# Kernel optimization log

Hardware: AMD Instinct MI355X
Metric: run time of the kernel (lower is better)

Reference implementation:

```python
import jax, jax.numpy as jnp
import numpy as np

N = 100000
E = 1600000
HID = 128
EPS = 1e-8


def _linear_params(key, fan_in, fan_out, bias=True, gain=1.0):
    kw, kb = jax.random.split(key)
    bound = gain / np.sqrt(fan_in)
    W = jax.random.uniform(kw, (fan_in, fan_out), jnp.float32, -bound, bound)
    if bias:
        b = jax.random.uniform(kb, (fan_out,), jnp.float32, -bound, bound)
        return W, b
    return W


def setup_inputs() -> dict:
    key = jax.random.key(0)
    ks = jax.random.split(key, 12)
    h = jax.random.normal(ks[0], (N, HID), jnp.float32)
    coord = jax.random.normal(ks[1], (N, 3), jnp.float32)
    edge_index = jax.random.randint(ks[2], (2, E), 0, N, jnp.int64)
    # edge_mlp: Linear(2*HID+1 -> HID), SiLU, Linear(HID -> HID), SiLU
    We1, be1 = _linear_params(ks[3], 2 * HID + 1, HID)
    We2, be2 = _linear_params(ks[4], HID, HID)
    # node_mlp: Linear(2*HID -> HID), SiLU, Linear(HID -> HID)
    Wn1, bn1 = _linear_params(ks[5], 2 * HID, HID)
    Wn2, bn2 = _linear_params(ks[6], HID, HID)
    # coord_mlp: Linear(HID -> HID), SiLU, Linear(HID -> 1, no bias, xavier gain=0.001)
    Wc1, bc1 = _linear_params(ks[7], HID, HID)
    Wc2 = _linear_params(ks[8], HID, 1, bias=False, gain=0.001 * np.sqrt(6.0 * HID / (HID + 1)))
    return {
        "h": h, "edge_index": edge_index, "coord": coord,
        "We1": We1, "be1": be1, "We2": We2, "be2": be2,
        "Wn1": Wn1, "bn1": bn1, "Wn2": Wn2, "bn2": bn2,
        "Wc1": Wc1, "bc1": bc1, "Wc2": Wc2,
    }


def _egcl(h, edge_index, coord, We1, be1, We2, be2, Wn1, bn1, Wn2, bn2, Wc1, bc1, Wc2):
    row, col = edge_index[0], edge_index[1]
    n = h.shape[0]
    # coord2radial (normalize=True, detach on norm)
    coord_diff = coord[row] - coord[col]                       # [E,3]
    radial = jnp.sum(coord_diff ** 2, axis=1, keepdims=True)   # [E,1]
    norm = jax.lax.stop_gradient(jnp.sqrt(radial)) + EPS
    coord_diff = coord_diff / norm
    # edge_model (no edge_attr, no attention)
    edge_in = jnp.concatenate([h[row], h[col], radial], axis=1)  # [E, 2H+1]
    m = jax.nn.silu(edge_in @ We1 + be1)
    m = jax.nn.silu(m @ We2 + be2)                               # [E,H]
    # coord_model (coords_agg='mean', tanh=False)
    phi_x = jax.nn.silu(m @ Wc1 + bc1) @ Wc2                     # [E,1]
    trans = coord_diff * phi_x                                   # [E,3]
    agg_c = jax.ops.segment_sum(trans, row, num_segments=n)
    cnt = jax.ops.segment_sum(jnp.ones((trans.shape[0],), trans.dtype), row, num_segments=n)
    agg_c = agg_c / jnp.clip(cnt, 1.0, None)[:, None]
    coord_out = coord + agg_c
    # node_model (residual=True)
    agg_h = jax.ops.segment_sum(m, row, num_segments=n)          # [N,H]
    node_in = jnp.concatenate([h, agg_h], axis=1)
    out = jax.nn.silu(node_in @ Wn1 + bn1) @ Wn2 + bn2
    h_out = h + out
    return h_out, coord_out


def reference(h, edge_index, coord, We1, be1, We2, be2, Wn1, bn1, Wn2, bn2, Wc1, bc1, Wc2):
    return _egcl(h, edge_index, coord, We1, be1, We2, be2, Wn1, bn1, Wn2, bn2, Wc1, bc1, Wc2)
```

## Files before the change

kernel.cpp:

```cpp
#include <hip/hip_runtime.h>

#define NN 100000
#define NE 1600000
#define HD 128
#define EPSV 1e-8f
#define EB 64
#define LPAD 136

typedef unsigned short ushort_t;
typedef __attribute__((ext_vector_type(8))) short bf16x8;
typedef __attribute__((ext_vector_type(4))) float f32x4;

__device__ __forceinline__ float silu_f(float x) {
    return x * __builtin_amdgcn_rcpf(1.0f + __expf(-x));
}
__device__ __forceinline__ float b2f(unsigned short u) {
    union { unsigned int i; float f; } v; v.i = ((unsigned int)u) << 16; return v.f;
}
__device__ __forceinline__ unsigned short f2b(float f) {
    union { float f; unsigned int i; } v; v.f = f;
    unsigned int r = v.i + 0x7fff + ((v.i >> 16) & 1);
    return (unsigned short)(r >> 16);
}
__device__ __forceinline__ unsigned int cvt_pk_bf16(float lo, float hi) {
    unsigned int r;
    asm("v_cvt_pk_bf16_f32 %0, %1, %2" : "=v"(r) : "v"(lo), "v"(hi));
    return r;
}
__device__ __forceinline__ bf16x8 frag_from_f32(const float* p) {
    float4 a0 = *(const float4*)p;
    float4 a1 = *(const float4*)(p + 4);
    union { bf16x8 v; uint4 u; } r;
    r.u.x = cvt_pk_bf16(a0.x, a0.y); r.u.y = cvt_pk_bf16(a0.z, a0.w);
    r.u.z = cvt_pk_bf16(a1.x, a1.y); r.u.w = cvt_pk_bf16(a1.z, a1.w);
    return r.v;
}

extern "C" __global__ __launch_bounds__(256)
void k_prep_hist(const int* __restrict__ ei, int* __restrict__ deg,
                 const float* __restrict__ We2, const float* __restrict__ Wc1,
                 const float* __restrict__ We1, const float* __restrict__ Wn1,
                 const float* __restrict__ Wn2,
                 ushort_t* __restrict__ We2T, ushort_t* __restrict__ Wc1T,
                 ushort_t* __restrict__ WabT, ushort_t* __restrict__ Wn1T,
                 ushort_t* __restrict__ Wn2T)
{
    int id = blockIdx.x * 256 + threadIdx.x;
    atomicAdd(&deg[ei[id]], 1);
    if (id < 16384) {
        int n = id >> 7, k = id & 127;
        We2T[id] = f2b(We2[k * HD + n]);
    } else if (id < 32768) {
        int r = id - 16384; int n = r >> 7, k = r & 127;
        Wc1T[r] = f2b(Wc1[k * HD + n]);
    } else if (id < 65536) {
        int r = id - 32768; int j = r >> 7, k = r & 127;
        float v = (j < 128) ? We1[k * HD + j] : We1[(size_t)(128 + k) * HD + (j - 128)];
        WabT[r] = f2b(v);
    } else if (id < 98304) {
        int r = id - 65536; int j = r >> 8, k = r & 255;
        Wn1T[r] = f2b(Wn1[(size_t)k * HD + j]);
    } else if (id < 114688) {
        int r = id - 98304; int j = r >> 7, k = r & 127;
        Wn2T[r] = f2b(Wn2[k * HD + j]);
    }
}

extern "C" __global__ __launch_bounds__(1024)
void k_scan1(const int* __restrict__ deg, int* __restrict__ bsum)
{
    __shared__ int wsum[16];
    const int tid = threadIdx.x;
    const int lane = tid & 63, w = tid >> 6;
    int i = blockIdx.x * 1024 + tid;
    int v = (i < NN) ? deg[i] : 0;
#pragma unroll
    for (int off = 32; off > 0; off >>= 1) v += __shfl_xor(v, off, 64);
    if (lane == 0) wsum[w] = v;
    __syncthreads();
    if (tid == 0) {
        int s = 0;
#pragma unroll
        for (int k = 0; k < 16; k++) s += wsum[k];
        bsum[blockIdx.x] = s;
    }
}

extern "C" __global__ __launch_bounds__(1024)
void k_scan3(const int* __restrict__ deg, const int* __restrict__ bsum,
             int* __restrict__ cursor)
{
    __shared__ int wsum[16];
    __shared__ int boff_s;
    const int tid = threadIdx.x;
    const int lane = tid & 63, w = tid >> 6;
    int i = blockIdx.x * 1024 + tid;
    int v = (i < NN) ? deg[i] : 0;
    int s = v;
#pragma unroll
    for (int off = 1; off < 64; off <<= 1) {
        int t = __shfl_up(s, off, 64);
        if (lane >= off) s += t;
    }
    if (lane == 63) wsum[w] = s;
    if (w == 0) {
        int a = 0;
        for (int k = lane; k < blockIdx.x; k += 64) a += bsum[k];
#pragma unroll
        for (int off = 32; off > 0; off >>= 1) a += __shfl_xor(a, off, 64);
        if (lane == 0) boff_s = a;
    }
    __syncthreads();
    if (w == 0) {
        int ws = (lane < 16) ? wsum[lane] : 0;
#pragma unroll
        for (int off = 1; off < 16; off <<= 1) {
            int t = __shfl_up(ws, off, 64);
            if (lane >= off) ws += t;
        }
        if (lane < 16) wsum[lane] = ws;
    }
    __syncthreads();
    int excl = boff_s + ((w > 0) ? wsum[w - 1] : 0) + s - v;
    if (i < NN) cursor[i] = excl;
}

extern "C" __global__ __launch_bounds__(256)
void k_sortids(const int* __restrict__ ei, int* __restrict__ cursor,
               int2* __restrict__ rc)
{
    int e = blockIdx.x * 256 + threadIdx.x;
    int r = ei[e], c = ei[NE + e];
    int slot = atomicAdd(&cursor[r], 1);
    rc[slot] = make_int2(r, c);
}

extern "C" __global__ __launch_bounds__(256)
void k_ab(const float* __restrict__ h, const ushort_t* __restrict__ WabT,
          const float* __restrict__ be1,
          ushort_t* __restrict__ A, ushort_t* __restrict__ B)
{
    const int tid = threadIdx.x;
    const int n0 = blockIdx.x * 64;
    const int wave = tid >> 6, lane = tid & 63;
    const int lr = lane & 15, lg = lane >> 4;
    const int node = n0 + wave * 16 + lr;
    const int nsrc = (node < NN) ? node : (NN - 1);

    f32x4 acc[16];
#pragma unroll
    for (int nt = 0; nt < 16; nt++) acc[nt] = (f32x4){0.f, 0.f, 0.f, 0.f};
#pragma unroll
    for (int ks = 0; ks < 4; ks++) {
        bf16x8 hf8 = frag_from_f32(h + (size_t)nsrc * HD + ks * 32 + lg * 8);
#pragma unroll
        for (int nt = 0; nt < 16; nt++) {
            bf16x8 wf = *(const bf16x8*)(WabT + (size_t)(nt * 16 + lr) * HD + ks * 32 + lg * 8);
            acc[nt] = __builtin_amdgcn_mfma_f32_16x16x32_bf16(wf, hf8, acc[nt], 0, 0, 0);
        }
    }
    if (node < NN) {
#pragma unroll
        for (int nt = 0; nt < 16; nt++) {
            float4 bias = (nt < 8) ? ((const float4*)be1)[nt * 4 + lg]
                                   : (float4){0.f, 0.f, 0.f, 0.f};
            uint2 pk;
            pk.x = cvt_pk_bf16(acc[nt][0] + bias.x, acc[nt][1] + bias.y);
            pk.y = cvt_pk_bf16(acc[nt][2] + bias.z, acc[nt][3] + bias.w);
            if (nt < 8)
                *(uint2*)(A + (size_t)node * HD + nt * 16 + lg * 4) = pk;
            else
                *(uint2*)(B + (size_t)node * HD + (nt - 8) * 16 + lg * 4) = pk;
        }
    }
}

extern "C" __global__ __launch_bounds__(256, 4)
void k_edge(const int2* __restrict__ rc, const float* __restrict__ coord,
            const ushort_t* __restrict__ A, const ushort_t* __restrict__ B,
            const float* __restrict__ WeL, const float* __restrict__ be2,
            const ushort_t* __restrict__ We2T,
            const ushort_t* __restrict__ Wc1T,
            const float* __restrict__ bc1, const float* __restrict__ Wc2,
            float* __restrict__ agg_h, float* __restrict__ agg_c)
{
    __shared__ ushort_t m_lds[EB][LPAD] __attribute__((aligned(16)));
    __shared__ float cd_lds[EB][3];
    __shared__ int rows_s[EB];
    __shared__ float bias_lds[384] __attribute__((aligned(16)));
    __shared__ float wel_lds[128] __attribute__((aligned(16)));

    const int tid = threadIdx.x;
    const int e  = tid >> 2;
    const int q  = tid & 3;
    const int wave = tid >> 6, lane = tid & 63;
    const int lr = lane & 15, lg = lane >> 4;

    if (tid < 128) { bias_lds[tid] = be2[tid]; bias_lds[256 + tid] = Wc2[tid]; }
    else           { bias_lds[tid] = bc1[tid - 128]; wel_lds[tid - 128] = WeL[tid - 128]; }

    int2 rce = rc[blockIdx.x * EB + e];
    const int row = rce.x, col = rce.y;

    float c0 = coord[(size_t)row * 3 + 0] - coord[(size_t)col * 3 + 0];
    float c1 = coord[(size_t)row * 3 + 1] - coord[(size_t)col * 3 + 1];
    float c2 = coord[(size_t)row * 3 + 2] - coord[(size_t)col * 3 + 2];
    float radial = c0 * c0 + c1 * c1 + c2 * c2;
    if (q == 0) {
        rows_s[e] = row;
        float inv = __builtin_amdgcn_rcpf(sqrtf(radial) + EPSV);
        cd_lds[e][0] = c0 * inv; cd_lds[e][1] = c1 * inv; cd_lds[e][2] = c2 * inv;
    }
    __syncthreads();

    {
        const bf16x8* A8 = (const bf16x8*)(A + (size_t)row * HD + q * 32);
        const bf16x8* B8 = (const bf16x8*)(B + (size_t)col * HD + q * 32);
        const float4* WL4 = (const float4*)wel_lds + q * 8;
#pragma unroll
        for (int i = 0; i < 4; i++) {
            bf16x8 av = A8[i], bv = B8[i];
            float4 w0 = WL4[2 * i], w1 = WL4[2 * i + 1];
            float v0 = silu_f(b2f((ushort_t)av[0]) + b2f((ushort_t)bv[0]) + radial * w0.x);
            float v1 = silu_f(b2f((ushort_t)av[1]) + b2f((ushort_t)bv[1]) + radial * w0.y);
            float v2 = silu_f(b2f((ushort_t)av[2]) + b2f((ushort_t)bv[2]) + radial * w0.z);
            float v3 = silu_f(b2f((ushort_t)av[3]) + b2f((ushort_t)bv[3]) + radial * w0.w);
            float v4 = silu_f(b2f((ushort_t)av[4]) + b2f((ushort_t)bv[4]) + radial * w1.x);
            float v5 = silu_f(b2f((ushort_t)av[5]) + b2f((ushort_t)bv[5]) + radial * w1.y);
            float v6 = silu_f(b2f((ushort_t)av[6]) + b2f((ushort_t)bv[6]) + radial * w1.z);
            float v7 = silu_f(b2f((ushort_t)av[7]) + b2f((ushort_t)bv[7]) + radial * w1.w);
            uint4 p;
            p.x = cvt_pk_bf16(v0, v1); p.y = cvt_pk_bf16(v2, v3);
            p.z = cvt_pk_bf16(v4, v5); p.w = cvt_pk_bf16(v6, v7);
            *(uint4*)&m_lds[e][q * 32 + i * 8] = p;
        }
    }
    __syncthreads();

    if (wave < 2) {
        f32x4 acc[2][8];
#pragma unroll
        for (int mt = 0; mt < 2; mt++)
#pragma unroll
            for (int nt = 0; nt < 8; nt++) acc[mt][nt] = (f32x4){0.f, 0.f, 0.f, 0.f};
#pragma unroll
        for (int ks = 0; ks < 4; ks++) {
            bf16x8 mf0 = *(const bf16x8*)&m_lds[wave * 32 + lr][ks * 32 + lg * 8];
            bf16x8 mf1 = *(const bf16x8*)&m_lds[wave * 32 + 16 + lr][ks * 32 + lg * 8];
#pragma unroll
            for (int nt = 0; nt < 8; nt++) {
                bf16x8 wf = *(const bf16x8*)(We2T + (size_t)(nt * 16 + lr) * HD + ks * 32 + lg * 8);
                acc[0][nt] = __builtin_amdgcn_mfma_f32_16x16x32_bf16(wf, mf0, acc[0][nt], 0, 0, 0);
                acc[1][nt] = __builtin_amdgcn_mfma_f32_16x16x32_bf16(wf, mf1, acc[1][nt], 0, 0, 0);
            }
        }
#pragma unroll
        for (int nt = 0; nt < 8; nt++) {
            float4 be2v = *(const float4*)&bias_lds[nt * 16 + lg * 4];
#pragma unroll
            for (int mt = 0; mt < 2; mt++) {
                float v0 = silu_f(acc[mt][nt][0] + be2v.x);
                float v1 = silu_f(acc[mt][nt][1] + be2v.y);
                float v2 = silu_f(acc[mt][nt][2] + be2v.z);
                float v3 = silu_f(acc[mt][nt][3] + be2v.w);
                uint2 pk; pk.x = cvt_pk_bf16(v0, v1); pk.y = cvt_pk_bf16(v2, v3);
                *(uint2*)&m_lds[wave * 32 + mt * 16 + lr][nt * 16 + lg * 4] = pk;
            }
        }

#pragma unroll
        for (int mt = 0; mt < 2; mt++)
#pragma unroll
            for (int nt = 0; nt < 8; nt++) acc[mt][nt] = (f32x4){0.f, 0.f, 0.f, 0.f};
#pragma unroll
        for (int ks = 0; ks < 4; ks++) {
            bf16x8 mf0 = *(const bf16x8*)&m_lds[wave * 32 + lr][ks * 32 + lg * 8];
            bf16x8 mf1 = *(const bf16x8*)&m_lds[wave * 32 + 16 + lr][ks * 32 + lg * 8];
#pragma unroll
            for (int nt = 0; nt < 8; nt++) {
                bf16x8 wf = *(const bf16x8*)(Wc1T + (size_t)(nt * 16 + lr) * HD + ks * 32 + lg * 8);
                acc[0][nt] = __builtin_amdgcn_mfma_f32_16x16x32_bf16(wf, mf0, acc[0][nt], 0, 0, 0);
                acc[1][nt] = __builtin_amdgcn_mfma_f32_16x16x32_bf16(wf, mf1, acc[1][nt], 0, 0, 0);
            }
        }

        float ph0 = 0.f, ph1 = 0.f;
#pragma unroll
        for (int nt = 0; nt < 8; nt++) {
            float4 bc1v = *(const float4*)&bias_lds[128 + nt * 16 + lg * 4];
            float4 wc2v = *(const float4*)&bias_lds[256 + nt * 16 + lg * 4];
            ph0 += silu_f(acc[0][nt][0] + bc1v.x) * wc2v.x
                 + silu_f(acc[0][nt][1] + bc1v.y) * wc2v.y
                 + silu_f(acc[0][nt][2] + bc1v.z) * wc2v.z
                 + silu_f(acc[0][nt][3] + bc1v.w) * wc2v.w;
            ph1 += silu_f(acc[1][nt][0] + bc1v.x) * wc2v.x
                 + silu_f(acc[1][nt][1] + bc1v.y) * wc2v.y
                 + silu_f(acc[1][nt][2] + bc1v.z) * wc2v.z
                 + silu_f(acc[1][nt][3] + bc1v.w) * wc2v.w;
        }
        ph0 += __shfl_xor(ph0, 16, 64); ph0 += __shfl_xor(ph0, 32, 64);
        ph1 += __shfl_xor(ph1, 16, 64); ph1 += __shfl_xor(ph1, 32, 64);
        if (lg == 0) {
            int e0 = wave * 32 + lr, e1 = e0 + 16;
            cd_lds[e0][0] *= ph0; cd_lds[e0][1] *= ph0; cd_lds[e0][2] *= ph0;
            cd_lds[e1][0] *= ph1; cd_lds[e1][1] *= ph1; cd_lds[e1][2] *= ph1;
        }
    }

    __syncthreads();

    {
        const int j = tid & 127, g = tid >> 7;
        const int es0 = g * 32, es1 = es0 + 32;
        float acc_r = 0.f;
        int cur = rows_s[es0];
        for (int es = es0; es < es1; es++) {
            int r = rows_s[es];
            if (r != cur) {
                atomicAdd(&agg_h[(size_t)cur * HD + j], acc_r);
                acc_r = 0.f; cur = r;
            }
            acc_r += b2f(m_lds[es][j]);
        }
        atomicAdd(&agg_h[(size_t)cur * HD + j], acc_r);
    }
    if (wave == 0) {
        int c = lane >> 4, sub = lane & 15;
        if (c < 3) {
            const int es0 = sub * 4, es1 = es0 + 4;
            float acc_r = 0.f;
            int cur = rows_s[es0];
            for (int es = es0; es < es1; es++) {
                int r = rows_s[es];
                if (r != cur) {
                    atomicAdd(&agg_c[(size_t)cur * 3 + c], acc_r);
                    acc_r = 0.f; cur = r;
                }
                acc_r += cd_lds[es][c];
            }
            atomicAdd(&agg_c[(size_t)cur * 3 + c], acc_r);
        }
    }
}

extern "C" __global__ __launch_bounds__(256)
void k_node(const float* __restrict__ h, const ushort_t* __restrict__ Wn1T,
            const float* __restrict__ bn1, const ushort_t* __restrict__ Wn2T,
            const float* __restrict__ bn2, const float* __restrict__ coord,
            const int* __restrict__ deg,
            float* __restrict__ hout ,
            float* __restrict__ cout )
{
    __shared__ ushort_t us[64][LPAD] __attribute__((aligned(16)));
    const int tid = threadIdx.x;
    const int n0 = blockIdx.x * 64;
    const int wave = tid >> 6, lane = tid & 63;
    const int lr = lane & 15, lg = lane >> 4;
    const int node = n0 + wave * 16 + lr;
    const int nsrc = (node < NN) ? node : (NN - 1);

    f32x4 acc[8];
#pragma unroll
    for (int nt = 0; nt < 8; nt++) acc[nt] = (f32x4){0.f, 0.f, 0.f, 0.f};
#pragma unroll
    for (int ks = 0; ks < 8; ks++) {
        const float* src = (ks < 4) ? (h + (size_t)nsrc * HD + ks * 32 + lg * 8)
                                    : (hout + (size_t)nsrc * HD + (ks - 4) * 32 + lg * 8);
        bf16x8 cf = frag_from_f32(src);
#pragma unroll
        for (int nt = 0; nt < 8; nt++) {
            bf16x8 wf = *(const bf16x8*)(Wn1T + (size_t)(nt * 16 + lr) * 256 + ks * 32 + lg * 8);
            acc[nt] = __builtin_amdgcn_mfma_f32_16x16x32_bf16(wf, cf, acc[nt], 0, 0, 0);
        }
    }
#pragma unroll
    for (int nt = 0; nt < 8; nt++) {
        float4 b1 = ((const float4*)bn1)[nt * 4 + lg];
        float v0 = silu_f(acc[nt][0] + b1.x);
        float v1 = silu_f(acc[nt][1] + b1.y);
        float v2 = silu_f(acc[nt][2] + b1.z);
        float v3 = silu_f(acc[nt][3] + b1.w);
        uint2 pk; pk.x = cvt_pk_bf16(v0, v1); pk.y = cvt_pk_bf16(v2, v3);
        *(uint2*)&us[wave * 16 + lr][nt * 16 + lg * 4] = pk;
    }

    f32x4 acc2[8];
#pragma unroll
    for (int nt = 0; nt < 8; nt++) acc2[nt] = (f32x4){0.f, 0.f, 0.f, 0.f};
#pragma unroll
    for (int ks = 0; ks < 4; ks++) {
        bf16x8 uf = *(const bf16x8*)&us[wave * 16 + lr][ks * 32 + lg * 8];
#pragma unroll
        for (int nt = 0; nt < 8; nt++) {
            bf16x8 wf = *(const bf16x8*)(Wn2T + (size_t)(nt * 16 + lr) * HD + ks * 32 + lg * 8);
            acc2[nt] = __builtin_amdgcn_mfma_f32_16x16x32_bf16(wf, uf, acc2[nt], 0, 0, 0);
        }
    }
    if (node < NN) {
#pragma unroll
        for (int nt = 0; nt < 8; nt++) {
            float4 b2 = ((const float4*)bn2)[nt * 4 + lg];
            size_t idx = (size_t)node * HD + nt * 16 + lg * 4;
            float4 hv = *(const float4*)(h + idx);
            float4 o;
            o.x = hv.x + acc2[nt][0] + b2.x;
            o.y = hv.y + acc2[nt][1] + b2.y;
            o.z = hv.z + acc2[nt][2] + b2.z;
            o.w = hv.w + acc2[nt][3] + b2.w;
            *(float4*)(hout + idx) = o;
        }
        if (lg == 0) {
            float invc = __builtin_amdgcn_rcpf(fmaxf((float)deg[node], 1.0f));
#pragma unroll
            for (int i = 0; i < 3; i++) {
                size_t idx = (size_t)node * 3 + i;
                cout[idx] = coord[idx] + cout[idx] * invc;
            }
        }
    }
}

extern "C" void kernel_launch(void* const* d_in, const int* in_sizes, int n_in,
                              void* d_out, int out_size, void* d_ws, size_t ws_size,
                              hipStream_t stream)
{
    const float* h     = (const float*)d_in[0];
    const int*   ei    = (const int*)d_in[1];
    const float* coord = (const float*)d_in[2];
    const float* We1   = (const float*)d_in[3];
    const float* be1   = (const float*)d_in[4];
    const float* We2   = (const float*)d_in[5];
    const float* be2   = (const float*)d_in[6];
    const float* Wn1   = (const float*)d_in[7];
    const float* bn1   = (const float*)d_in[8];
    const float* Wn2   = (const float*)d_in[9];
    const float* bn2   = (const float*)d_in[10];
    const float* Wc1   = (const float*)d_in[11];
    const float* bc1   = (const float*)d_in[12];
    const float* Wc2   = (const float*)d_in[13];

    float* out   = (float*)d_out;
    float* agg_h = out;
    float* agg_c = out + (size_t)NN * HD;

    ushort_t* A    = (ushort_t*)d_ws;
    ushort_t* B    = A + (size_t)NN * HD;
    ushort_t* We2T = B + (size_t)NN * HD;
    ushort_t* Wc1T = We2T + 16384;
    ushort_t* WabT = Wc1T + 16384;
    ushort_t* Wn1T = WabT + 32768;
    ushort_t* Wn2T = Wn1T + 32768;
    int* deg    = (int*)(Wn2T + 16384);
    int* cursor = deg + NN;
    int* bsum   = cursor + NN;
    int2* rc    = (int2*)(bsum + 128);
    const float* WeL = We1 + (size_t)2 * HD * HD;

    const int scan_nb = (NN + 1023) / 1024;

    hipMemsetAsync(d_out, 0, (size_t)out_size * sizeof(float), stream);
    hipMemsetAsync(deg, 0, (size_t)NN * sizeof(int), stream);

    k_prep_hist<<<NE / 256, 256, 0, stream>>>(ei, deg, We2, Wc1, We1, Wn1, Wn2,
                                              We2T, Wc1T, WabT, Wn1T, Wn2T);
    k_ab<<<(NN + 63) / 64, 256, 0, stream>>>(h, WabT, be1, A, B);
    k_scan1<<<scan_nb, 1024, 0, stream>>>(deg, bsum);
    k_scan3<<<scan_nb, 1024, 0, stream>>>(deg, bsum, cursor);
    k_sortids<<<NE / 256, 256, 0, stream>>>(ei, cursor, rc);
    k_edge<<<NE / EB, 256, 0, stream>>>(rc, coord, A, B, WeL, be2,
                                        We2T, Wc1T, bc1, Wc2, agg_h, agg_c);
    k_node<<<(NN + 63) / 64, 256, 0, stream>>>(h, Wn1T, bn1, Wn2T, bn2, coord,
                                               deg, agg_h, agg_c);
}
```

Baseline: 961.6 us.

## Shrink edge kernel to 128 threads and K-chunk the edge MLP through half-width LDS

k_edge now runs 128 threads per block instead of 256, so both waves perform the MFMA work; previously only two of the four waves did the matmuls. The first-layer activations are built and consumed in two 64-wide K chunks, and the second-layer output is split between LDS and registers. This halves the m_lds tile (padded stride 72 instead of 136), and the agg_h atomics are done in two halves with extra barriers. The aim is to cut idle waves and LDS footprint so more blocks fit per CU, at the cost of extra synchronisation, more register pressure from holding half of m in registers, and twice as many reduction passes.

```diff
diff --git a/kernel.cpp b/kernel.cpp
--- a/kernel.cpp
+++ b/kernel.cpp
@@ -5,6 +5,7 @@
 #define HD 128
 #define EPSV 1e-8f
 #define EB 64
+#define LP2 72
 #define LPAD 136
 
 typedef unsigned short ushort_t;
@@ -175,7 +176,7 @@
     }
 }
 
-extern "C" __global__ __launch_bounds__(256, 4)
+extern "C" __global__ __launch_bounds__(128, 5)
 void k_edge(const int2* __restrict__ rc, const float* __restrict__ coord,
             const ushort_t* __restrict__ A, const ushort_t* __restrict__ B,
             const float* __restrict__ WeL, const float* __restrict__ be2,
@@ -184,20 +185,22 @@
             const float* __restrict__ bc1, const float* __restrict__ Wc2,
             float* __restrict__ agg_h, float* __restrict__ agg_c)
 {
-    __shared__ ushort_t m_lds[EB][LPAD] __attribute__((aligned(16)));
+    __shared__ ushort_t m_lds[EB][LP2] __attribute__((aligned(16)));
     __shared__ float cd_lds[EB][3];
     __shared__ int rows_s[EB];
     __shared__ float bias_lds[384] __attribute__((aligned(16)));
     __shared__ float wel_lds[128] __attribute__((aligned(16)));
 
     const int tid = threadIdx.x;
-    const int e  = tid >> 2;
-    const int q  = tid & 3;
+    const int e  = tid >> 1;
+    const int hf = tid & 1;
     const int wave = tid >> 6, lane = tid & 63;
     const int lr = lane & 15, lg = lane >> 4;
 
-    if (tid < 128) { bias_lds[tid] = be2[tid]; bias_lds[256 + tid] = Wc2[tid]; }
-    else           { bias_lds[tid] = bc1[tid - 128]; wel_lds[tid - 128] = WeL[tid - 128]; }
+    bias_lds[tid]       = be2[tid];
+    bias_lds[128 + tid] = bc1[tid];
+    bias_lds[256 + tid] = Wc2[tid];
+    wel_lds[tid] = WeL[tid];
 
     int2 rce = rc[blockIdx.x * EB + e];
     const int row = rce.x, col = rce.y;
@@ -206,111 +209,98 @@
     float c1 = coord[(size_t)row * 3 + 1] - coord[(size_t)col * 3 + 1];
     float c2 = coord[(size_t)row * 3 + 2] - coord[(size_t)col * 3 + 2];
     float radial = c0 * c0 + c1 * c1 + c2 * c2;
-    if (q == 0) {
+    if (hf == 0) {
         rows_s[e] = row;
         float inv = __builtin_amdgcn_rcpf(sqrtf(radial) + EPSV);
         cd_lds[e][0] = c0 * inv; cd_lds[e][1] = c1 * inv; cd_lds[e][2] = c2 * inv;
     }
     __syncthreads();
 
-    {
-        const bf16x8* A8 = (const bf16x8*)(A + (size_t)row * HD + q * 32);
-        const bf16x8* B8 = (const bf16x8*)(B + (size_t)col * HD + q * 32);
-        const float4* WL4 = (const float4*)wel_lds + q * 8;
-#pragma unroll
-        for (int i = 0; i < 4; i++) {
-            bf16x8 av = A8[i], bv = B8[i];
-            float4 w0 = WL4[2 * i], w1 = WL4[2 * i + 1];
-            float v0 = silu_f(b2f((ushort_t)av[0]) + b2f((ushort_t)bv[0]) + radial * w0.x);
-            float v1 = silu_f(b2f((ushort_t)av[1]) + b2f((ushort_t)bv[1]) + radial * w0.y);
-            float v2 = silu_f(b2f((ushort_t)av[2]) + b2f((ushort_t)bv[2]) + radial * w0.z);
-            float v3 = silu_f(b2f((ushort_t)av[3]) + b2f((ushort_t)bv[3]) + radial * w0.w);
-            float v4 = silu_f(b2f((ushort_t)av[4]) + b2f((ushort_t)bv[4]) + radial * w1.x);
-            float v5 = silu_f(b2f((ushort_t)av[5]) + b2f((ushort_t)bv[5]) + radial * w1.y);
-            float v6 = silu_f(b2f((ushort_t)av[6]) + b2f((ushort_t)bv[6]) + radial * w1.z);
-            float v7 = silu_f(b2f((ushort_t)av[7]) + b2f((ushort_t)bv[7]) + radial * w1.w);
-            uint4 p;
-            p.x = cvt_pk_bf16(v0, v1); p.y = cvt_pk_bf16(v2, v3);
-            p.z = cvt_pk_bf16(v4, v5); p.w = cvt_pk_bf16(v6, v7);
-            *(uint4*)&m_lds[e][q * 32 + i * 8] = p;
-        }
-    }
-    __syncthreads();
-
-    if (wave < 2) {
-        f32x4 acc[2][8];
-#pragma unroll
-        for (int mt = 0; mt < 2; mt++)
-#pragma unroll
-            for (int nt = 0; nt < 8; nt++) acc[mt][nt] = (f32x4){0.f, 0.f, 0.f, 0.f};
-#pragma unroll
-        for (int ks = 0; ks < 4; ks++) {
+    const ushort_t* Arow = A + (size_t)row * HD;
+    const ushort_t* Brow = B + (size_t)col * HD;
+
+    f32x4 acc[2][8];
+#pragma unroll
+    for (int mt = 0; mt < 2; mt++)
+#pragma unroll
+        for (int nt = 0; nt < 8; nt++) acc[mt][nt] = (f32x4){0.f, 0.f, 0.f, 0.f};
+
+#pragma unroll
+    for (int kc = 0; kc < 2; kc++) {
+        const int kb = kc * 64;
+        {
+            const bf16x8* A8 = (const bf16x8*)(Arow + kb + hf * 32);
+            const bf16x8* B8 = (const bf16x8*)(Brow + kb + hf * 32);
+            const float4* WL4 = (const float4*)wel_lds + kb / 4 + hf * 8;
+#pragma unroll
+            for (int i = 0; i < 4; i++) {
+                bf16x8 av = A8[i], bv = B8[i];
+                float4 w0 = WL4[2 * i], w1 = WL4[2 * i + 1];
+                float v0 = silu_f(b2f((ushort_t)av[0]) + b2f((ushort_t)bv[0]) + radial * w0.x);
+                float v1 = silu_f(b2f((ushort_t)av[1]) + b2f((ushort_t)bv[1]) + radial * w0.y);
+                float v2 = silu_f(b2f((ushort_t)av[2]) + b2f((ushort_t)bv[2]) + radial * w0.z);
+                float v3 = silu_f(b2f((ushort_t)av[3]) + b2f((ushort_t)bv[3]) + radial * w0.w);
+                float v4 = silu_f(b2f((ushort_t)av[4]) + b2f((ushort_t)bv[4]) + radial * w1.x);
+                float v5 = silu_f(b2f((ushort_t)av[5]) + b2f((ushort_t)bv[5]) + radial * w1.y);
+                float v6 = silu_f(b2f((ushort_t)av[6]) + b2f((ushort_t)bv[6]) + radial * w1.z);
+                float v7 = silu_f(b2f((ushort_t)av[7]) + b2f((ushort_t)bv[7]) + radial * w1.w);
+                uint4 p;
+                p.x = cvt_pk_bf16(v0, v1); p.y = cvt_pk_bf16(v2, v3);
+                p.z = cvt_pk_bf16(v4, v5); p.w = cvt_pk_bf16(v6, v7);
+                *(uint4*)&m_lds[e][hf * 32 + i * 8] = p;
+            }
+        }
+#pragma unroll
+        for (int ks = 0; ks < 2; ks++) {
             bf16x8 mf0 = *(const bf16x8*)&m_lds[wave * 32 + lr][ks * 32 + lg * 8];
             bf16x8 mf1 = *(const bf16x8*)&m_lds[wave * 32 + 16 + lr][ks * 32 + lg * 8];
 #pragma unroll
             for (int nt = 0; nt < 8; nt++) {
-                bf16x8 wf = *(const bf16x8*)(We2T + (size_t)(nt * 16 + lr) * HD + ks * 32 + lg * 8);
+                bf16x8 wf = *(const bf16x8*)(We2T + (size_t)(nt * 16 + lr) * HD + kb + ks * 32 + lg * 8);
                 acc[0][nt] = __builtin_amdgcn_mfma_f32_16x16x32_bf16(wf, mf0, acc[0][nt], 0, 0, 0);
                 acc[1][nt] = __builtin_amdgcn_mfma_f32_16x16x32_bf16(wf, mf1, acc[1][nt], 0, 0, 0);
             }
         }
+    }
+
+    uint2 mreg[2][4];
+#pragma unroll
+    for (int nt = 0; nt < 8; nt++) {
+        float4 be2v = *(const float4*)&bias_lds[nt * 16 + lg * 4];
+#pragma unroll
+        for (int mt = 0; mt < 2; mt++) {
+            float v0 = silu_f(acc[mt][nt][0] + be2v.x);
+            float v1 = silu_f(acc[mt][nt][1] + be2v.y);
+            float v2 = silu_f(acc[mt][nt][2] + be2v.z);
+            float v3 = silu_f(acc[mt][nt][3] + be2v.w);
+            uint2 pk; pk.x = cvt_pk_bf16(v0, v1); pk.y = cvt_pk_bf16(v2, v3);
+            if (nt < 4)
+                *(uint2*)&m_lds[wave * 32 + mt * 16 + lr][nt * 16 + lg * 4] = pk;
+            else
+                mreg[mt][nt - 4] = pk;
+        }
+    }
+
+#pragma unroll
+    for (int mt = 0; mt < 2; mt++)
+#pragma unroll
+        for (int nt = 0; nt < 8; nt++) acc[mt][nt] = (f32x4){0.f, 0.f, 0.f, 0.f};
+#pragma unroll
+    for (int ks = 0; ks < 2; ks++) {
+        bf16x8 mf0 = *(const bf16x8*)&m_lds[wave * 32 + lr][ks * 32 + lg * 8];
+        bf16x8 mf1 = *(const bf16x8*)&m_lds[wave * 32 + 16 + lr][ks * 32 + lg * 8];
 #pragma unroll
         for (int nt = 0; nt < 8; nt++) {
-            float4 be2v = *(const float4*)&bias_lds[nt * 16 + lg * 4];
-#pragma unroll
-            for (int mt = 0; mt < 2; mt++) {
-                float v0 = silu_f(acc[mt][nt][0] + be2v.x);
-                float v1 = silu_f(acc[mt][nt][1] + be2v.y);
-                float v2 = silu_f(acc[mt][nt][2] + be2v.z);
-                float v3 = silu_f(acc[mt][nt][3] + be2v.w);
-                uint2 pk; pk.x = cvt_pk_bf16(v0, v1); pk.y = cvt_pk_bf16(v2, v3);
-                *(uint2*)&m_lds[wave * 32 + mt * 16 + lr][nt * 16 + lg * 4] = pk;
-            }
-        }
-
-#pragma unroll
-        for (int mt = 0; mt < 2; mt++)
-#pragma unroll
-            for (int nt = 0; nt < 8; nt++) acc[mt][nt] = (f32x4){0.f, 0.f, 0.f, 0.f};
-#pragma unroll
-        for (int ks = 0; ks < 4; ks++) {
-            bf16x8 mf0 = *(const bf16x8*)&m_lds[wave * 32 + lr][ks * 32 + lg * 8];
-            bf16x8 mf1 = *(const bf16x8*)&m_lds[wave * 32 + 16 + lr][ks * 32 + lg * 8];
-#pragma unroll
-            for (int nt = 0; nt < 8; nt++) {
-                bf16x8 wf = *(const bf16x8*)(Wc1T + (size_t)(nt * 16 + lr) * HD + ks * 32 + lg * 8);
-                acc[0][nt] = __builtin_amdgcn_mfma_f32_16x16x32_bf16(wf, mf0, acc[0][nt], 0, 0, 0);
-                acc[1][nt] = __builtin_amdgcn_mfma_f32_16x16x32_bf16(wf, mf1, acc[1][nt], 0, 0, 0);
-            }
-        }
-
-        float ph0 = 0.f, ph1 = 0.f;
-#pragma unroll
-        for (int nt = 0; nt < 8; nt++) {
-            float4 bc1v = *(const float4*)&bias_lds[128 + nt * 16 + lg * 4];
-            float4 wc2v = *(const float4*)&bias_lds[256 + nt * 16 + lg * 4];
-            ph0 += silu_f(acc[0][nt][0] + bc1v.x) * wc2v.x
-                 + silu_f(acc[0][nt][1] + bc1v.y) * wc2v.y
-                 + silu_f(acc[0][nt][2] + bc1v.z) * wc2v.z
-                 + silu_f(acc[0][nt][3] + bc1v.w) * wc2v.w;
-            ph1 += silu_f(acc[1][nt][0] + bc1v.x) * wc2v.x
-                 + silu_f(acc[1][nt][1] + bc1v.y) * wc2v.y
-                 + silu_f(acc[1][nt][2] + bc1v.z) * wc2v.z
-                 + silu_f(acc[1][nt][3] + bc1v.w) * wc2v.w;
-        }
-        ph0 += __shfl_xor(ph0, 16, 64); ph0 += __shfl_xor(ph0, 32, 64);
-        ph1 += __shfl_xor(ph1, 16, 64); ph1 += __shfl_xor(ph1, 32, 64);
-        if (lg == 0) {
-            int e0 = wave * 32 + lr, e1 = e0 + 16;
-            cd_lds[e0][0] *= ph0; cd_lds[e0][1] *= ph0; cd_lds[e0][2] *= ph0;
-            cd_lds[e1][0] *= ph1; cd_lds[e1][1] *= ph1; cd_lds[e1][2] *= ph1;
+            bf16x8 wf = *(const bf16x8*)(Wc1T + (size_t)(nt * 16 + lr) * HD + ks * 32 + lg * 8);
+            acc[0][nt] = __builtin_amdgcn_mfma_f32_16x16x32_bf16(wf, mf0, acc[0][nt], 0, 0, 0);
+            acc[1][nt] = __builtin_amdgcn_mfma_f32_16x16x32_bf16(wf, mf1, acc[1][nt], 0, 0, 0);
         }
     }
 
     __syncthreads();
 
     {
-        const int j = tid & 127, g = tid >> 7;
+        const int j = tid & 63, g = tid >> 6;
         const int es0 = g * 32, es1 = es0 + 32;
         float acc_r = 0.f;
         int cur = rows_s[es0];
@@ -323,6 +313,66 @@
             acc_r += b2f(m_lds[es][j]);
         }
         atomicAdd(&agg_h[(size_t)cur * HD + j], acc_r);
+    }
+
+    __syncthreads();
+
+#pragma unroll
+    for (int nt4 = 0; nt4 < 4; nt4++)
+#pragma unroll
+        for (int mt = 0; mt < 2; mt++)
+            *(uint2*)&m_lds[wave * 32 + mt * 16 + lr][nt4 * 16 + lg * 4] = mreg[mt][nt4];
+
+#pragma unroll
+    for (int ks = 0; ks < 2; ks++) {
+        bf16x8 mf0 = *(const bf16x8*)&m_lds[wave * 32 + lr][ks * 32 + lg * 8];
+        bf16x8 mf1 = *(const bf16x8*)&m_lds[wave * 32 + 16 + lr][ks * 32 + lg * 8];
+#pragma unroll
+        for (int nt = 0; nt < 8; nt++) {
+            bf16x8 wf = *(const bf16x8*)(Wc1T + (size_t)(nt * 16 + lr) * HD + 64 + ks * 32 + lg * 8);
+            acc[0][nt] = __builtin_amdgcn_mfma_f32_16x16x32_bf16(wf, mf0, acc[0][nt], 0, 0, 0);
+            acc[1][nt] = __builtin_amdgcn_mfma_f32_16x16x32_bf16(wf, mf1, acc[1][nt], 0, 0, 0);
+        }
+    }
+
+    float ph0 = 0.f, ph1 = 0.f;
+#pragma unroll
+    for (int nt = 0; nt < 8; nt++) {
+        float4 bc1v = *(const float4*)&bias_lds[128 + nt * 16 + lg * 4];
+        float4 wc2v = *(const float4*)&bias_lds[256 + nt * 16 + lg * 4];
+        ph0 += silu_f(acc[0][nt][0] + bc1v.x) * wc2v.x
+             + silu_f(acc[0][nt][1] + bc1v.y) * wc2v.y
+             + silu_f(acc[0][nt][2] + bc1v.z) * wc2v.z
+             + silu_f(acc[0][nt][3] + bc1v.w) * wc2v.w;
+        ph1 += silu_f(acc[1][nt][0] + bc1v.x) * wc2v.x
+             + silu_f(acc[1][nt][1] + bc1v.y) * wc2v.y
+             + silu_f(acc[1][nt][2] + bc1v.z) * wc2v.z
+             + silu_f(acc[1][nt][3] + bc1v.w) * wc2v.w;
+    }
+    ph0 += __shfl_xor(ph0, 16, 64); ph0 += __shfl_xor(ph0, 32, 64);
+    ph1 += __shfl_xor(ph1, 16, 64); ph1 += __shfl_xor(ph1, 32, 64);
+    if (lg == 0) {
+        int e0 = wave * 32 + lr, e1 = e0 + 16;
+        cd_lds[e0][0] *= ph0; cd_lds[e0][1] *= ph0; cd_lds[e0][2] *= ph0;
+        cd_lds[e1][0] *= ph1; cd_lds[e1][1] *= ph1; cd_lds[e1][2] *= ph1;
+    }
+
+    __syncthreads();
+
+    {
+        const int j = tid & 63, g = tid >> 6;
+        const int es0 = g * 32, es1 = es0 + 32;
+        float acc_r = 0.f;
+        int cur = rows_s[es0];
+        for (int es = es0; es < es1; es++) {
+            int r = rows_s[es];
+            if (r != cur) {
+                atomicAdd(&agg_h[(size_t)cur * HD + 64 + j], acc_r);
+                acc_r = 0.f; cur = r;
+            }
+            acc_r += b2f(m_lds[es][j]);
+        }
+        atomicAdd(&agg_h[(size_t)cur * HD + 64 + j], acc_r);
     }
     if (wave == 0) {
         int c = lane >> 4, sub = lane & 15;
@@ -467,7 +517,7 @@
     k_scan1<<<scan_nb, 1024, 0, stream>>>(deg, bsum);
     k_scan3<<<scan_nb, 1024, 0, stream>>>(deg, bsum, cursor);
     k_sortids<<<NE / 256, 256, 0, stream>>>(ei, cursor, rc);
-    k_edge<<<NE / EB, 256, 0, stream>>>(rc, coord, A, B, WeL, be2,
+    k_edge<<<NE / EB, 128, 0, stream>>>(rc, coord, A, B, WeL, be2,
                                         We2T, Wc1T, bc1, Wc2, agg_h, agg_c);
     k_node<<<(NN + 63) / 64, 256, 0, stream>>>(h, Wn1T, bn1, Wn2T, bn2, coord,
                                                deg, agg_h, agg_c);
```

Result: slower. 1.290 ms (+34.1%).
